# Optimization experiments

Hardware: AMD Instinct MI355X
Metric: run time of the kernel (lower is better)

The kernel has to match this reference:

```python
import jax, jax.numpy as jnp
import numpy as np

N_NODES = 50000


def gcn_conv(h, W, b, src, dst, n_nodes):
    # PyG GCNConv: h' = D^{-1/2} (A + I) D^{-1/2} (h @ W) + b
    h = h @ W  # [N, out]
    deg = jax.ops.segment_sum(jnp.ones_like(dst, dtype=h.dtype), dst, num_segments=n_nodes)
    dinv = jnp.where(deg > 0, jax.lax.rsqrt(deg), 0.0)  # [N]
    norm = dinv[src] * dinv[dst]  # [E]
    msg = h[src] * norm[:, None]  # [E, out]
    out = jax.ops.segment_sum(msg, dst, num_segments=n_nodes)
    return out + b


def setup_inputs() -> dict:
    key = jax.random.key(0)
    ks = jax.random.split(key, 12)
    N, E, P, D, H = N_NODES, 1600000, 200000, 128, 128
    s = lambda fan_in: 1.0 / np.sqrt(fan_in)
    return {
        "x": jax.random.normal(ks[0], (N, D), dtype=jnp.float32),
        "edge_index": jax.random.randint(ks[1], (2, E), 0, N, dtype=jnp.int32),
        "drug_pairs": jax.random.randint(ks[2], (P, 2), 0, N, dtype=jnp.int32),
        "W1": jax.random.normal(ks[3], (D, H), dtype=jnp.float32) * s(D),
        "b1": jnp.zeros((H,), dtype=jnp.float32),
        "W2": jax.random.normal(ks[4], (H, H), dtype=jnp.float32) * s(H),
        "b2": jnp.zeros((H,), dtype=jnp.float32),
        "Wh1": jax.random.normal(ks[5], (2 * H, H), dtype=jnp.float32) * s(2 * H),
        "bh1": jnp.zeros((H,), dtype=jnp.float32),
        "Wh2": jax.random.normal(ks[6], (H, 1), dtype=jnp.float32) * s(H),
        "bh2": jnp.zeros((1,), dtype=jnp.float32),
    }


def reference(x, edge_index, drug_pairs, W1, b1, W2, b2, Wh1, bh1, Wh2, bh2):
    n = x.shape[0]
    # add self-loops once (GCNConv default add_self_loops=True)
    loop = jnp.arange(n, dtype=edge_index.dtype)
    src = jnp.concatenate([edge_index[0], loop])
    dst = jnp.concatenate([edge_index[1], loop])

    h = jax.nn.relu(gcn_conv(x, W1, b1, src, dst, n))  # dropout = identity (eval)
    h = jax.nn.relu(gcn_conv(h, W2, b2, src, dst, n))

    combined = jnp.concatenate([h[drug_pairs[:, 0]], h[drug_pairs[:, 1]]], axis=1)  # [P, 2H]
    out = jax.nn.relu(combined @ Wh1 + bh1) @ Wh2 + bh2  # [P, 1]
    return out
```

## Files before the change

kernel.cpp:

```cpp
#include <hip/hip_runtime.h>
#include <hip/hip_fp16.h>


#define BSH 9
#define BSZ (1 << BSH)
#define MSB 4096
#define XPAD 132
#define HB 256

typedef __attribute__((ext_vector_type(8))) short bf16x8;
typedef __attribute__((ext_vector_type(8))) _Float16 f16x8;
typedef __attribute__((ext_vector_type(4))) float f32x4;

__device__ __forceinline__ void acc8(uint4 u, float4& lo, float4& hi) {
  float2 f0 = __half22float2(((const __half2*)&u)[0]);
  float2 f1 = __half22float2(((const __half2*)&u)[1]);
  float2 f2 = __half22float2(((const __half2*)&u)[2]);
  float2 f3 = __half22float2(((const __half2*)&u)[3]);
  lo.x += f0.x; lo.y += f0.y; lo.z += f1.x; lo.w += f1.y;
  hi.x += f2.x; hi.y += f2.y; hi.z += f3.x; hi.w += f3.y;
}

__device__ __forceinline__ void split8(const float* v, bf16x8& hi, bf16x8& lo) {
#pragma unroll
  for (int j = 0; j < 8; ++j) {
    unsigned u = __float_as_uint(v[j]);
    hi[j] = (short)(u >> 16);
    float lf = v[j] - __uint_as_float(u & 0xffff0000u);
    lo[j] = (short)(__float_as_uint(lf) >> 16);
  }
}

__global__ __launch_bounds__(256) void k_prep_hist(
    const float* __restrict__ W1, const float* __restrict__ W2,
    const float* __restrict__ Wh1, short* __restrict__ fragH,
    short* __restrict__ fragL,
    const int* __restrict__ dst, int* __restrict__ gcnt, int e, int kb) {
  if (blockIdx.x >= 32) {
    __shared__ int h4[512];
    int bid = blockIdx.x - 32;
    int tid = threadIdx.x, wid = tid >> 6;
    for (int t = tid; t < 512; t += 256) h4[t] = 0;
    __syncthreads();
    for (int i = bid * 256 + tid; i < e; i += HB * 256) {
      int d = __builtin_nontemporal_load(&dst[i]);
      atomicAdd(&h4[wid * 128 + (d >> BSH)], 1);
    }
    __syncthreads();
    if (tid < kb)
      atomicAdd(&gcnt[tid], h4[tid] + h4[128 + tid] + h4[256 + tid] + h4[384 + tid]);
    return;
  }
  int g = blockIdx.x * 256 + threadIdx.x;
  int w = g >> 11;
  int rem = g & 2047;
  int lane = rem & 63;
  int ts = rem >> 6;
  int t = ts >> 2, s = ts & 3;
  int n = (t << 4) + (lane & 15);
  int k0 = s * 32 + (lane >> 4) * 8;
  const float* W = (w == 0) ? W1 : (w == 1) ? W2 : (w == 2) ? Wh1 : (Wh1 + 128 * 128);
  short h[8], l[8];
#pragma unroll
  for (int j = 0; j < 8; ++j) {
    float x = W[(k0 + j) * 128 + n];
    if (w == 0) {
      unsigned u = __float_as_uint(x);
      h[j] = (short)(u >> 16);
      float lf = x - __uint_as_float(u & 0xffff0000u);
      l[j] = (short)(__float_as_uint(lf) >> 16);
    } else {
      __half hh = __float2half(x);
      h[j] = __half_as_short(hh);
      l[j] = __half_as_short(__float2half(x - __half2float(hh)));
    }
  }
  ((int4*)fragH)[g] = *(int4*)h;
  ((int4*)fragL)[g] = *(int4*)l;
}

__global__ __launch_bounds__(256) void k_gemm_mfma(
    const float* __restrict__ X, const short* __restrict__ fragH,
    const short* __restrict__ fragL, const float* __restrict__ rowscale,
    __half* __restrict__ C16, int n) {
  __shared__ float sX[64 * XPAD];
  int tid = threadIdx.x;
  int row0 = blockIdx.x * 64;
  const float2* X2 = (const float2*)(X + (size_t)row0 * 128);
#pragma unroll
  for (int it = 0; it < 16; ++it) {
    int t = it * 256 + tid;
    int r = t >> 6, c2 = t & 63;
    int gr = row0 + r;
    float2 v = (gr < n) ? X2[t] : make_float2(0.f, 0.f);
    *(float2*)&sX[r * XPAD + c2 * 2] = v;
  }
  __syncthreads();
  int wid = tid >> 6, lane = tid & 63;
  int r0 = row0 + wid * 16;
  if (r0 >= n) return;
  int m = lane & 15, quad = lane >> 4;
  const float* xrow = sX + (wid * 16 + m) * XPAD;
  f32x4 acc[8];
#pragma unroll
  for (int t = 0; t < 8; ++t) acc[t] = (f32x4)(0.f);
  const int4* FH = (const int4*)fragH;
  const int4* FL = (const int4*)fragL;
#pragma unroll
  for (int s = 0; s < 4; ++s) {
    int k0 = s * 32 + quad * 8;
    float xv[8];
    *(float2*)&xv[0] = *(const float2*)(xrow + k0);
    *(float2*)&xv[2] = *(const float2*)(xrow + k0 + 2);
    *(float2*)&xv[4] = *(const float2*)(xrow + k0 + 4);
    *(float2*)&xv[6] = *(const float2*)(xrow + k0 + 6);
    bf16x8 ah, al;
    split8(xv, ah, al);
#pragma unroll
    for (int t = 0; t < 8; ++t) {
      int idx = (t * 4 + s) * 64 + lane;
      bf16x8 bh = *(const bf16x8*)&FH[idx];
      bf16x8 bl = *(const bf16x8*)&FL[idx];
      acc[t] = __builtin_amdgcn_mfma_f32_16x16x32_bf16(ah, bh, acc[t], 0, 0, 0);
      acc[t] = __builtin_amdgcn_mfma_f32_16x16x32_bf16(al, bh, acc[t], 0, 0, 0);
      acc[t] = __builtin_amdgcn_mfma_f32_16x16x32_bf16(ah, bl, acc[t], 0, 0, 0);
    }
  }
  float sc[4];
#pragma unroll
  for (int r = 0; r < 4; ++r)
    sc[r] = rowscale[r0 + quad * 4 + r];
#pragma unroll
  for (int t = 0; t < 8; ++t) {
#pragma unroll
    for (int r = 0; r < 4; ++r) {
      int row = r0 + quad * 4 + r;
      C16[(size_t)row * 128 + t * 16 + m] = __float2half(acc[t][r] * sc[r]);
    }
  }
}

__global__ __launch_bounds__(256) void k_gemm_f16(
    const __half* __restrict__ X16, const short* __restrict__ fragH,
    const short* __restrict__ fragL, const float* __restrict__ rowscale,
    __half* __restrict__ C16, int n) {
  int wid = threadIdx.x >> 6, lane = threadIdx.x & 63;
  int r0 = (blockIdx.x * 4 + wid) * 16;
  if (r0 >= n) return;
  int m = lane & 15, quad = lane >> 4;
  const uint4* Xr = (const uint4*)(X16 + (size_t)(r0 + m) * 128);
  f32x4 acc[8];
#pragma unroll
  for (int t = 0; t < 8; ++t) acc[t] = (f32x4)(0.f);
  const int4* FH = (const int4*)fragH;
  const int4* FL = (const int4*)fragL;
#pragma unroll
  for (int s = 0; s < 4; ++s) {
    uint4 av = Xr[quad + 4 * s];
    f16x8 a = *(const f16x8*)&av;
#pragma unroll
    for (int t = 0; t < 8; ++t) {
      int idx = (t * 4 + s) * 64 + lane;
      int4 bhv = FH[idx], blv = FL[idx];
      f16x8 bh = *(const f16x8*)&bhv;
      f16x8 bl = *(const f16x8*)&blv;
      acc[t] = __builtin_amdgcn_mfma_f32_16x16x32_f16(a, bh, acc[t], 0, 0, 0);
      acc[t] = __builtin_amdgcn_mfma_f32_16x16x32_f16(a, bl, acc[t], 0, 0, 0);
    }
  }
  float sc[4];
#pragma unroll
  for (int r = 0; r < 4; ++r)
    sc[r] = rowscale ? rowscale[r0 + quad * 4 + r] : 1.f;
#pragma unroll
  for (int t = 0; t < 8; ++t) {
#pragma unroll
    for (int r = 0; r < 4; ++r) {
      int row = r0 + quad * 4 + r;
      C16[(size_t)row * 128 + t * 16 + m] = __float2half(acc[t][r] * sc[r]);
    }
  }
}

__global__ __launch_bounds__(256) void k_gemm_dual_f16(
    const __half* __restrict__ X16,
    const short* __restrict__ fHa, const short* __restrict__ fLa,
    const short* __restrict__ fHb, const short* __restrict__ fLb,
    __half* __restrict__ A16, __half* __restrict__ B16, int n) {
  int wid = threadIdx.x >> 6, lane = threadIdx.x & 63;
  int r0 = (blockIdx.x * 4 + wid) * 16;
  if (r0 >= n) return;
  int m = lane & 15, quad = lane >> 4;
  const uint4* Xr = (const uint4*)(X16 + (size_t)(r0 + m) * 128);
  f32x4 accA[8], accB[8];
#pragma unroll
  for (int t = 0; t < 8; ++t) { accA[t] = (f32x4)(0.f); accB[t] = (f32x4)(0.f); }
  const int4* FHa = (const int4*)fHa; const int4* FLa = (const int4*)fLa;
  const int4* FHb = (const int4*)fHb; const int4* FLb = (const int4*)fLb;
#pragma unroll
  for (int s = 0; s < 4; ++s) {
    uint4 av = Xr[quad + 4 * s];
    f16x8 a = *(const f16x8*)&av;
#pragma unroll
    for (int t = 0; t < 8; ++t) {
      int idx = (t * 4 + s) * 64 + lane;
      int4 v0 = FHa[idx], v1 = FLa[idx], v2 = FHb[idx], v3 = FLb[idx];
      accA[t] = __builtin_amdgcn_mfma_f32_16x16x32_f16(a, *(const f16x8*)&v0, accA[t], 0, 0, 0);
      accA[t] = __builtin_amdgcn_mfma_f32_16x16x32_f16(a, *(const f16x8*)&v1, accA[t], 0, 0, 0);
      accB[t] = __builtin_amdgcn_mfma_f32_16x16x32_f16(a, *(const f16x8*)&v2, accB[t], 0, 0, 0);
      accB[t] = __builtin_amdgcn_mfma_f32_16x16x32_f16(a, *(const f16x8*)&v3, accB[t], 0, 0, 0);
    }
  }
#pragma unroll
  for (int t = 0; t < 8; ++t) {
#pragma unroll
    for (int r = 0; r < 4; ++r) {
      int row = r0 + quad * 4 + r;
      A16[(size_t)row * 128 + t * 16 + m] = __float2half(accA[t][r]);
      B16[(size_t)row * 128 + t * 16 + m] = __float2half(accB[t][r]);
    }
  }
}

__global__ __launch_bounds__(256) void k_multisplit(const int* __restrict__ src,
                                                    const int* __restrict__ dst,
                                                    const int* __restrict__ gcnt,
                                                    int* __restrict__ gcur,
                                                    int* __restrict__ tmp,
                                                    int e, int kb) {
  __shared__ int h4[4 * 128], off[4 * 128], sbase[128], ws[2];
  int tid = threadIdx.x, wid = tid >> 6, lane = tid & 63;
  for (int t = tid; t < 512; t += 256) h4[t] = 0;
  __syncthreads();
  int i0 = blockIdx.x * MSB + tid;
  int d[16], rk[16];
#pragma unroll
  for (int u = 0; u < 16; ++u) {
    int i = i0 + u * 256;
    if (i < e) {
      d[u] = __builtin_nontemporal_load(&dst[i]);
      rk[u] = atomicAdd(&h4[wid * 128 + (d[u] >> BSH)], 1);
    }
  }
  __syncthreads();
  int tot = 0;
  if (tid < 128) {
    int c0 = h4[tid], c1 = h4[128 + tid], c2 = h4[256 + tid], c3 = h4[384 + tid];
    off[tid] = 0; off[128 + tid] = c0;
    off[256 + tid] = c0 + c1; off[384 + tid] = c0 + c1 + c2;
    tot = c0 + c1 + c2 + c3;
  }
  int v = (tid < 128 && tid < kb) ? gcnt[tid] : 0;
  int orig = v;
#pragma unroll
  for (int o = 1; o < 64; o <<= 1) {
    int u = __shfl_up(v, o, 64);
    if (lane >= o) v += u;
  }
  if (lane == 63 && wid < 2) ws[wid] = v;
  __syncthreads();
  if (tid < 128) sbase[tid] = ((wid == 1) ? ws[0] : 0) + v - orig;
  __syncthreads();
  if (tid < kb && tot > 0) sbase[tid] += atomicAdd(&gcur[tid], tot);
  __syncthreads();
#pragma unroll
  for (int u = 0; u < 16; ++u) {
    int i = i0 + u * 256;
    if (i < e) {
      int s = __builtin_nontemporal_load(&src[i]);
      int k = d[u] >> BSH;
      tmp[sbase[k] + off[wid * 128 + k] + rk[u]] = ((d[u] & (BSZ - 1)) << 16) | s;
    }
  }
}

__global__ __launch_bounds__(512) void k_bucket_build(
    const int* __restrict__ tmp, const int* __restrict__ gcnt,
    int* __restrict__ rowptr, float* __restrict__ dinv,
    unsigned short* __restrict__ colarr, int n, int kb, int e) {
  __shared__ int dl[BSZ], cl[BSZ], sbase[128], ws[8];
  int t = threadIdx.x, b = blockIdx.x;
  int lane = t & 63, w = t >> 6;
  int v = (t < 128 && t < kb) ? gcnt[t] : 0;
  int orig0 = v;
#pragma unroll
  for (int o = 1; o < 64; o <<= 1) {
    int u = __shfl_up(v, o, 64);
    if (lane >= o) v += u;
  }
  if (lane == 63 && w < 2) ws[w] = v;
  dl[t] = 0;
  __syncthreads();
  if (t < 128) sbase[t] = ((w == 1) ? ws[0] : 0) + v - orig0;
  __syncthreads();
  int s0 = sbase[b];
  int s1 = s0 + gcnt[b];
  for (int j = s0 + t; j < s1; j += 512)
    atomicAdd(&dl[((unsigned)tmp[j]) >> 16], 1);
  __syncthreads();
  int dv = dl[t], orig = dv;
#pragma unroll
  for (int o = 1; o < 64; o <<= 1) {
    int u = __shfl_up(dv, o, 64);
    if (lane >= o) dv += u;
  }
  if (lane == 63) ws[w] = dv;
  __syncthreads();
  if (t == 0) {
    int a = 0;
#pragma unroll
    for (int k = 0; k < 8; ++k) { int x = ws[k]; ws[k] = a; a += x; }
  }
  __syncthreads();
  int ex = ws[w] + dv - orig;
  cl[t] = ex;
  int node = (b << BSH) + t;
  if (node < n) {
    rowptr[node] = s0 + ex;
    dinv[node] = rsqrtf((float)(orig + 1));
  }
  if (b == kb - 1 && t == 0) rowptr[n] = e;
  __syncthreads();
  for (int j = s0 + t; j < s1; j += 512) {
    int p = tmp[j];
    int r = atomicAdd(&cl[((unsigned)p) >> 16], 1);
    colarr[s0 + r] = (unsigned short)(p & 0xFFFF);
  }
}

__global__ __launch_bounds__(256) void k_agg_h(
    const __half2* __restrict__ g2, const float* __restrict__ dinv,
    const int* __restrict__ rowptr, const unsigned short* __restrict__ col,
    const float* __restrict__ bias, __half* __restrict__ out16, int n) {
  int i = blockIdx.x * 4 + (threadIdx.x >> 6);
  if (i >= n) return;
  int lane = threadIdx.x & 63;
  int sub = lane >> 4;
  int c8 = lane & 15;
  const uint4* G = (const uint4*)g2;
  float4 z = make_float4(0.f, 0.f, 0.f, 0.f);
  float4 lo0 = z, lo1 = z, lo2 = z, lo3 = z, hi0 = z, hi1 = z, hi2 = z, hi3 = z;
  if (sub == 0) acc8(G[(size_t)i * 16 + c8], lo0, hi0);
  int beg = rowptr[i], end = rowptr[i + 1];
  int j = beg;
  for (; j + 16 <= end; j += 16) {
    int s0 = __builtin_nontemporal_load(&col[j + sub]);
    int s1 = __builtin_nontemporal_load(&col[j + 4 + sub]);
    int s2 = __builtin_nontemporal_load(&col[j + 8 + sub]);
    int s3 = __builtin_nontemporal_load(&col[j + 12 + sub]);
    uint4 u0 = G[(size_t)s0 * 16 + c8];
    uint4 u1 = G[(size_t)s1 * 16 + c8];
    uint4 u2 = G[(size_t)s2 * 16 + c8];
    uint4 u3 = G[(size_t)s3 * 16 + c8];
    acc8(u0, lo0, hi0); acc8(u1, lo1, hi1);
    acc8(u2, lo2, hi2); acc8(u3, lo3, hi3);
  }
  for (; j + 4 <= end; j += 4) {
    int s0 = __builtin_nontemporal_load(&col[j + sub]);
    acc8(G[(size_t)s0 * 16 + c8], lo1, hi1);
  }
  int rem = end - j;
  if (sub < rem) {
    int s0 = __builtin_nontemporal_load(&col[j + sub]);
    acc8(G[(size_t)s0 * 16 + c8], lo2, hi2);
  }
  float4 lo, hi;
  lo.x = (lo0.x + lo1.x) + (lo2.x + lo3.x);
  lo.y = (lo0.y + lo1.y) + (lo2.y + lo3.y);
  lo.z = (lo0.z + lo1.z) + (lo2.z + lo3.z);
  lo.w = (lo0.w + lo1.w) + (lo2.w + lo3.w);
  hi.x = (hi0.x + hi1.x) + (hi2.x + hi3.x);
  hi.y = (hi0.y + hi1.y) + (hi2.y + hi3.y);
  hi.z = (hi0.z + hi1.z) + (hi2.z + hi3.z);
  hi.w = (hi0.w + hi1.w) + (hi2.w + hi3.w);
  lo.x += __shfl_down(lo.x, 32, 64); lo.x += __shfl_down(lo.x, 16, 64);
  lo.y += __shfl_down(lo.y, 32, 64); lo.y += __shfl_down(lo.y, 16, 64);
  lo.z += __shfl_down(lo.z, 32, 64); lo.z += __shfl_down(lo.z, 16, 64);
  lo.w += __shfl_down(lo.w, 32, 64); lo.w += __shfl_down(lo.w, 16, 64);
  hi.x += __shfl_down(hi.x, 32, 64); hi.x += __shfl_down(hi.x, 16, 64);
  hi.y += __shfl_down(hi.y, 32, 64); hi.y += __shfl_down(hi.y, 16, 64);
  hi.z += __shfl_down(hi.z, 32, 64); hi.z += __shfl_down(hi.z, 16, 64);
  hi.w += __shfl_down(hi.w, 32, 64); hi.w += __shfl_down(hi.w, 16, 64);
  if (sub == 0) {
    float di = dinv[i];
    float4 b0 = ((const float4*)bias)[2 * c8];
    float4 b1 = ((const float4*)bias)[2 * c8 + 1];
    __half2 q0 = __floats2half2_rn(fmaxf(fmaf(di, lo.x, b0.x), 0.f),
                                   fmaxf(fmaf(di, lo.y, b0.y), 0.f));
    __half2 q1 = __floats2half2_rn(fmaxf(fmaf(di, lo.z, b0.z), 0.f),
                                   fmaxf(fmaf(di, lo.w, b0.w), 0.f));
    __half2 q2 = __floats2half2_rn(fmaxf(fmaf(di, hi.x, b1.x), 0.f),
                                   fmaxf(fmaf(di, hi.y, b1.y), 0.f));
    __half2 q3 = __floats2half2_rn(fmaxf(fmaf(di, hi.z, b1.z), 0.f),
                                   fmaxf(fmaf(di, hi.w, b1.w), 0.f));
    uint4 o;
    o.x = *(unsigned*)&q0; o.y = *(unsigned*)&q1;
    o.z = *(unsigned*)&q2; o.w = *(unsigned*)&q3;
    ((uint4*)out16)[(size_t)i * 16 + c8] = o;
  }
}

__global__ __launch_bounds__(256) void k_pairs_h(
    const __half* __restrict__ A, const __half* __restrict__ B,
    const int* __restrict__ pairs, const float* __restrict__ bh1,
    const float* __restrict__ wh2, const float* __restrict__ bh2,
    float* __restrict__ out, int P) {
  int wp = (blockIdx.x * 4 + (threadIdx.x >> 6)) * 4;
  int lane = threadIdx.x & 63;
  int sub = lane >> 4;
  int c8 = lane & 15;
  int pr = sub >> 1;
  int ab = sub & 1;
  const uint4* T = ab ? (const uint4*)B : (const uint4*)A;
  int pA = wp + pr;
  int pB = wp + 2 + pr;
  uint4 u0 = make_uint4(0, 0, 0, 0), u1 = u0;
  if (pA < P) {
    int r = pairs[2 * pA + ab];
    u0 = T[(size_t)r * 16 + c8];
  }
  if (pB < P) {
    int r = pairs[2 * pB + ab];
    u1 = T[(size_t)r * 16 + c8];
  }
  float4 b0 = ((const float4*)bh1)[2 * c8];
  float4 b1 = ((const float4*)bh1)[2 * c8 + 1];
  float4 w0 = ((const float4*)wh2)[2 * c8];
  float4 w1 = ((const float4*)wh2)[2 * c8 + 1];
  float s0, s1;
  {
    float4 lo = make_float4(0, 0, 0, 0), hi = lo;
    acc8(u0, lo, hi);
    lo.x += __shfl_down(lo.x, 16, 64); lo.y += __shfl_down(lo.y, 16, 64);
    lo.z += __shfl_down(lo.z, 16, 64); lo.w += __shfl_down(lo.w, 16, 64);
    hi.x += __shfl_down(hi.x, 16, 64); hi.y += __shfl_down(hi.y, 16, 64);
    hi.z += __shfl_down(hi.z, 16, 64); hi.w += __shfl_down(hi.w, 16, 64);
    s0 = fmaxf(lo.x + b0.x, 0.f) * w0.x + fmaxf(lo.y + b0.y, 0.f) * w0.y +
         fmaxf(lo.z + b0.z, 0.f) * w0.z + fmaxf(lo.w + b0.w, 0.f) * w0.w +
         fmaxf(hi.x + b1.x, 0.f) * w1.x + fmaxf(hi.y + b1.y, 0.f) * w1.y +
         fmaxf(hi.z + b1.z, 0.f) * w1.z + fmaxf(hi.w + b1.w, 0.f) * w1.w;
  }
  {
    float4 lo = make_float4(0, 0, 0, 0), hi = lo;
    acc8(u1, lo, hi);
    lo.x += __shfl_down(lo.x, 16, 64); lo.y += __shfl_down(lo.y, 16, 64);
    lo.z += __shfl_down(lo.z, 16, 64); lo.w += __shfl_down(lo.w, 16, 64);
    hi.x += __shfl_down(hi.x, 16, 64); hi.y += __shfl_down(hi.y, 16, 64);
    hi.z += __shfl_down(hi.z, 16, 64); hi.w += __shfl_down(hi.w, 16, 64);
    s1 = fmaxf(lo.x + b0.x, 0.f) * w0.x + fmaxf(lo.y + b0.y, 0.f) * w0.y +
         fmaxf(lo.z + b0.z, 0.f) * w0.z + fmaxf(lo.w + b0.w, 0.f) * w0.w +
         fmaxf(hi.x + b1.x, 0.f) * w1.x + fmaxf(hi.y + b1.y, 0.f) * w1.y +
         fmaxf(hi.z + b1.z, 0.f) * w1.z + fmaxf(hi.w + b1.w, 0.f) * w1.w;
  }
#pragma unroll
  for (int o = 8; o > 0; o >>= 1) {
    s0 += __shfl_down(s0, o, 64);
    s1 += __shfl_down(s1, o, 64);
  }
  float bb = bh2[0];
  if (lane == 0 && wp < P) out[wp] = s0 + bb;
  if (lane == 32 && wp + 1 < P) out[wp + 1] = s0 + bb;
  if (lane == 0 && wp + 2 < P) out[wp + 2] = s1 + bb;
  if (lane == 32 && wp + 3 < P) out[wp + 3] = s1 + bb;
}

extern "C" void kernel_launch(void* const* d_in, const int* in_sizes, int n_in,
                              void* d_out, int out_size, void* d_ws, size_t ws_size,
                              hipStream_t stream) {
  const float* x   = (const float*)d_in[0];
  const int* ei    = (const int*)d_in[1];
  const int* pairs = (const int*)d_in[2];
  const float* W1  = (const float*)d_in[3];
  const float* b1  = (const float*)d_in[4];
  const float* W2  = (const float*)d_in[5];
  const float* b2  = (const float*)d_in[6];
  const float* Wh1 = (const float*)d_in[7];
  const float* bh1 = (const float*)d_in[8];
  const float* Wh2 = (const float*)d_in[9];
  const float* bh2 = (const float*)d_in[10];
  (void)n_in; (void)out_size; (void)ws_size;

  int N = in_sizes[0] / 128;
  int E = in_sizes[1] / 2;
  int P = in_sizes[2] / 2;
  const int* src = ei;
  const int* dst = ei + E;
  int KB = (N + BSZ - 1) >> BSH;

  char* wsp = (char*)d_ws;
  size_t off = 0;
  auto alloc = [&](size_t bytes) -> void* {
    void* p = wsp + off;
    off += (bytes + 255) & ~(size_t)255;
    return p;
  };
  __half* g16 = (__half*)alloc((size_t)N * 128 * 2);
  __half* h1  = (__half*)alloc((size_t)N * 128 * 2);
  __half* h2  = (__half*)alloc((size_t)N * 128 * 2);
  float* dinv = (float*)alloc((size_t)N * 4);
  int* rowptr = (int*)alloc((size_t)(N + 1) * 4);
  unsigned short* colarr = (unsigned short*)alloc((size_t)E * 2);
  int* tmp    = (int*)alloc((size_t)E * 4);
  short* fragH = (short*)alloc(4 * 2048 * 8 * 2);
  short* fragL = (short*)alloc(4 * 2048 * 8 * 2);
  int* gcnt  = (int*)alloc((size_t)(KB + 1) * 4);
  int* gcur  = (int*)alloc((size_t)(KB + 1) * 4);
  __half* A16 = g16;
  __half* B16 = h1;
  short* fH_W1 = fragH + 0 * 16384;  short* fL_W1 = fragL + 0 * 16384;
  short* fH_W2 = fragH + 1 * 16384;  short* fL_W2 = fragL + 1 * 16384;
  short* fH_Wa = fragH + 2 * 16384;  short* fL_Wa = fragL + 2 * 16384;
  short* fH_Wb = fragH + 3 * 16384;  short* fL_Wb = fragL + 3 * 16384;

  int GB = (N + 63) / 64;
  int GF = (N / 16 + 3) / 4;
  int AB = (N + 3) / 4;

  hipMemsetAsync(gcnt, 0, (size_t)(KB + 1) * 4, stream);
  hipMemsetAsync(gcur, 0, (size_t)(KB + 1) * 4, stream);
  k_prep_hist<<<32 + HB, 256, 0, stream>>>(W1, W2, Wh1, fragH, fragL,
                                           dst, gcnt, E, KB);
  k_multisplit<<<(E + MSB - 1) / MSB, 256, 0, stream>>>(src, dst, gcnt, gcur,
                                                        tmp, E, KB);
  k_bucket_build<<<KB, 512, 0, stream>>>(tmp, gcnt, rowptr, dinv, colarr, N, KB, E);
  k_gemm_mfma<<<GB, 256, 0, stream>>>(x, fH_W1, fL_W1, dinv, g16, N);
  k_agg_h<<<AB, 256, 0, stream>>>((const __half2*)g16, dinv, rowptr, colarr, b1, h1, N);
  k_gemm_f16<<<GF, 256, 0, stream>>>(h1, fH_W2, fL_W2, dinv, g16, N);
  k_agg_h<<<AB, 256, 0, stream>>>((const __half2*)g16, dinv, rowptr, colarr, b2, h2, N);
  k_gemm_dual_f16<<<GF, 256, 0, stream>>>(h2, fH_Wa, fL_Wa, fH_Wb, fL_Wb,
                                          A16, B16, N);
  k_pairs_h<<<(P + 15) / 16, 256, 0, stream>>>(A16, B16, pairs, bh1, Wh2, bh2,
                                               (float*)d_out, P);
}
```

Before: 353.2 us.

## Co-launch multisplit with first GEMM and apply dinv scaling in separate pass

Merges the edge multisplit kernel and the first-layer GEMM into one launch, with the block index choosing which body runs, so the GEMM no longer waits for the CSR build. Because dinv is not yet known at GEMM time, the row scaling moves to a new elementwise kernel that runs after the bucket build. The GEMM writes its output in fp16 before scaling and the new pass rounds it again, which can change numerics slightly. The extra pass also rereads and rewrites the 50000x128 fp16 buffer, and the two memsets are merged into one.

```diff
diff --git a/kernel.cpp b/kernel.cpp
--- a/kernel.cpp
+++ b/kernel.cpp
@@ -79,13 +79,12 @@
   ((int4*)fragL)[g] = *(int4*)l;
 }
 
-__global__ __launch_bounds__(256) void k_gemm_mfma(
+__device__ __forceinline__ void gemm1_body(
     const float* __restrict__ X, const short* __restrict__ fragH,
-    const short* __restrict__ fragL, const float* __restrict__ rowscale,
-    __half* __restrict__ C16, int n) {
-  __shared__ float sX[64 * XPAD];
+    const short* __restrict__ fragL, __half* __restrict__ C16, int n,
+    int bid, float* sX) {
   int tid = threadIdx.x;
-  int row0 = blockIdx.x * 64;
+  int row0 = bid * 64;
   const float2* X2 = (const float2*)(X + (size_t)row0 * 128);
 #pragma unroll
   for (int it = 0; it < 16; ++it) {
@@ -126,18 +125,151 @@
       acc[t] = __builtin_amdgcn_mfma_f32_16x16x32_bf16(ah, bl, acc[t], 0, 0, 0);
     }
   }
-  float sc[4];
-#pragma unroll
-  for (int r = 0; r < 4; ++r)
-    sc[r] = rowscale[r0 + quad * 4 + r];
 #pragma unroll
   for (int t = 0; t < 8; ++t) {
 #pragma unroll
     for (int r = 0; r < 4; ++r) {
       int row = r0 + quad * 4 + r;
-      C16[(size_t)row * 128 + t * 16 + m] = __float2half(acc[t][r] * sc[r]);
-    }
-  }
+      C16[(size_t)row * 128 + t * 16 + m] = __float2half(acc[t][r]);
+    }
+  }
+}
+
+__device__ __forceinline__ void multisplit_body(
+    const int* __restrict__ src, const int* __restrict__ dst,
+    const int* __restrict__ gcnt, int* __restrict__ gcur,
+    int* __restrict__ tmp, int e, int kb, int bid, int* lds) {
+  int* h4 = lds;
+  int* off = lds + 512;
+  int* sbase = lds + 1024;
+  int* ws = lds + 1152;
+  int tid = threadIdx.x, wid = tid >> 6, lane = tid & 63;
+  for (int t = tid; t < 512; t += 256) h4[t] = 0;
+  __syncthreads();
+  int i0 = bid * MSB + tid;
+  int d[16], rk[16];
+#pragma unroll
+  for (int u = 0; u < 16; ++u) {
+    int i = i0 + u * 256;
+    if (i < e) {
+      d[u] = __builtin_nontemporal_load(&dst[i]);
+      rk[u] = atomicAdd(&h4[wid * 128 + (d[u] >> BSH)], 1);
+    }
+  }
+  __syncthreads();
+  int tot = 0;
+  if (tid < 128) {
+    int c0 = h4[tid], c1 = h4[128 + tid], c2 = h4[256 + tid], c3 = h4[384 + tid];
+    off[tid] = 0; off[128 + tid] = c0;
+    off[256 + tid] = c0 + c1; off[384 + tid] = c0 + c1 + c2;
+    tot = c0 + c1 + c2 + c3;
+  }
+  int v = (tid < 128 && tid < kb) ? gcnt[tid] : 0;
+  int orig = v;
+#pragma unroll
+  for (int o = 1; o < 64; o <<= 1) {
+    int u = __shfl_up(v, o, 64);
+    if (lane >= o) v += u;
+  }
+  if (lane == 63 && wid < 2) ws[wid] = v;
+  __syncthreads();
+  if (tid < 128) sbase[tid] = ((wid == 1) ? ws[0] : 0) + v - orig;
+  __syncthreads();
+  if (tid < kb && tot > 0) sbase[tid] += atomicAdd(&gcur[tid], tot);
+  __syncthreads();
+#pragma unroll
+  for (int u = 0; u < 16; ++u) {
+    int i = i0 + u * 256;
+    if (i < e) {
+      int s = __builtin_nontemporal_load(&src[i]);
+      int k = d[u] >> BSH;
+      tmp[sbase[k] + off[wid * 128 + k] + rk[u]] = ((d[u] & (BSZ - 1)) << 16) | s;
+    }
+  }
+}
+
+__global__ __launch_bounds__(256) void k_ms_gemm1(
+    const int* __restrict__ src, const int* __restrict__ dst,
+    const int* __restrict__ gcnt, int* __restrict__ gcur,
+    int* __restrict__ tmp, int e, int kb, int msblocks,
+    const float* __restrict__ X, const short* __restrict__ fragH,
+    const short* __restrict__ fragL, __half* __restrict__ C16, int n) {
+  __shared__ float sX[64 * XPAD];
+  if ((int)blockIdx.x < msblocks) {
+    multisplit_body(src, dst, gcnt, gcur, tmp, e, kb, blockIdx.x, (int*)sX);
+    return;
+  }
+  gemm1_body(X, fragH, fragL, C16, n, blockIdx.x - msblocks, sX);
+}
+
+__global__ __launch_bounds__(512) void k_bucket_build(
+    const int* __restrict__ tmp, const int* __restrict__ gcnt,
+    int* __restrict__ rowptr, float* __restrict__ dinv,
+    unsigned short* __restrict__ colarr, int n, int kb, int e) {
+  __shared__ int dl[BSZ], cl[BSZ], sbase[128], ws[8];
+  int t = threadIdx.x, b = blockIdx.x;
+  int lane = t & 63, w = t >> 6;
+  int v = (t < 128 && t < kb) ? gcnt[t] : 0;
+  int orig0 = v;
+#pragma unroll
+  for (int o = 1; o < 64; o <<= 1) {
+    int u = __shfl_up(v, o, 64);
+    if (lane >= o) v += u;
+  }
+  if (lane == 63 && w < 2) ws[w] = v;
+  dl[t] = 0;
+  __syncthreads();
+  if (t < 128) sbase[t] = ((w == 1) ? ws[0] : 0) + v - orig0;
+  __syncthreads();
+  int s0 = sbase[b];
+  int s1 = s0 + gcnt[b];
+  for (int j = s0 + t; j < s1; j += 512)
+    atomicAdd(&dl[((unsigned)tmp[j]) >> 16], 1);
+  __syncthreads();
+  int dv = dl[t], orig = dv;
+#pragma unroll
+  for (int o = 1; o < 64; o <<= 1) {
+    int u = __shfl_up(dv, o, 64);
+    if (lane >= o) dv += u;
+  }
+  if (lane == 63) ws[w] = dv;
+  __syncthreads();
+  if (t == 0) {
+    int a = 0;
+#pragma unroll
+    for (int k = 0; k < 8; ++k) { int x = ws[k]; ws[k] = a; a += x; }
+  }
+  __syncthreads();
+  int ex = ws[w] + dv - orig;
+  cl[t] = ex;
+  int node = (b << BSH) + t;
+  if (node < n) {
+    rowptr[node] = s0 + ex;
+    dinv[node] = rsqrtf((float)(orig + 1));
+  }
+  if (b == kb - 1 && t == 0) rowptr[n] = e;
+  __syncthreads();
+  for (int j = s0 + t; j < s1; j += 512) {
+    int p = tmp[j];
+    int r = atomicAdd(&cl[((unsigned)p) >> 16], 1);
+    colarr[s0 + r] = (unsigned short)(p & 0xFFFF);
+  }
+}
+
+__global__ __launch_bounds__(256) void k_gscale(__half* __restrict__ g16,
+                                                const float* __restrict__ dinv,
+                                                int n) {
+  int idx = blockIdx.x * 256 + threadIdx.x;
+  if (idx >= n * 16) return;
+  float di = dinv[idx >> 4];
+  uint4 u = ((const uint4*)g16)[idx];
+  __half2* hp = (__half2*)&u;
+#pragma unroll
+  for (int k = 0; k < 4; ++k) {
+    float2 f = __half22float2(hp[k]);
+    hp[k] = __floats2half2_rn(f.x * di, f.y * di);
+  }
+  ((uint4*)g16)[idx] = u;
 }
 
 __global__ __launch_bounds__(256) void k_gemm_f16(
@@ -219,112 +351,6 @@
       A16[(size_t)row * 128 + t * 16 + m] = __float2half(accA[t][r]);
       B16[(size_t)row * 128 + t * 16 + m] = __float2half(accB[t][r]);
     }
-  }
-}
-
-__global__ __launch_bounds__(256) void k_multisplit(const int* __restrict__ src,
-                                                    const int* __restrict__ dst,
-                                                    const int* __restrict__ gcnt,
-                                                    int* __restrict__ gcur,
-                                                    int* __restrict__ tmp,
-                                                    int e, int kb) {
-  __shared__ int h4[4 * 128], off[4 * 128], sbase[128], ws[2];
-  int tid = threadIdx.x, wid = tid >> 6, lane = tid & 63;
-  for (int t = tid; t < 512; t += 256) h4[t] = 0;
-  __syncthreads();
-  int i0 = blockIdx.x * MSB + tid;
-  int d[16], rk[16];
-#pragma unroll
-  for (int u = 0; u < 16; ++u) {
-    int i = i0 + u * 256;
-    if (i < e) {
-      d[u] = __builtin_nontemporal_load(&dst[i]);
-      rk[u] = atomicAdd(&h4[wid * 128 + (d[u] >> BSH)], 1);
-    }
-  }
-  __syncthreads();
-  int tot = 0;
-  if (tid < 128) {
-    int c0 = h4[tid], c1 = h4[128 + tid], c2 = h4[256 + tid], c3 = h4[384 + tid];
-    off[tid] = 0; off[128 + tid] = c0;
-    off[256 + tid] = c0 + c1; off[384 + tid] = c0 + c1 + c2;
-    tot = c0 + c1 + c2 + c3;
-  }
-  int v = (tid < 128 && tid < kb) ? gcnt[tid] : 0;
-  int orig = v;
-#pragma unroll
-  for (int o = 1; o < 64; o <<= 1) {
-    int u = __shfl_up(v, o, 64);
-    if (lane >= o) v += u;
-  }
-  if (lane == 63 && wid < 2) ws[wid] = v;
-  __syncthreads();
-  if (tid < 128) sbase[tid] = ((wid == 1) ? ws[0] : 0) + v - orig;
-  __syncthreads();
-  if (tid < kb && tot > 0) sbase[tid] += atomicAdd(&gcur[tid], tot);
-  __syncthreads();
-#pragma unroll
-  for (int u = 0; u < 16; ++u) {
-    int i = i0 + u * 256;
-    if (i < e) {
-      int s = __builtin_nontemporal_load(&src[i]);
-      int k = d[u] >> BSH;
-      tmp[sbase[k] + off[wid * 128 + k] + rk[u]] = ((d[u] & (BSZ - 1)) << 16) | s;
-    }
-  }
-}
-
-__global__ __launch_bounds__(512) void k_bucket_build(
-    const int* __restrict__ tmp, const int* __restrict__ gcnt,
-    int* __restrict__ rowptr, float* __restrict__ dinv,
-    unsigned short* __restrict__ colarr, int n, int kb, int e) {
-  __shared__ int dl[BSZ], cl[BSZ], sbase[128], ws[8];
-  int t = threadIdx.x, b = blockIdx.x;
-  int lane = t & 63, w = t >> 6;
-  int v = (t < 128 && t < kb) ? gcnt[t] : 0;
-  int orig0 = v;
-#pragma unroll
-  for (int o = 1; o < 64; o <<= 1) {
-    int u = __shfl_up(v, o, 64);
-    if (lane >= o) v += u;
-  }
-  if (lane == 63 && w < 2) ws[w] = v;
-  dl[t] = 0;
-  __syncthreads();
-  if (t < 128) sbase[t] = ((w == 1) ? ws[0] : 0) + v - orig0;
-  __syncthreads();
-  int s0 = sbase[b];
-  int s1 = s0 + gcnt[b];
-  for (int j = s0 + t; j < s1; j += 512)
-    atomicAdd(&dl[((unsigned)tmp[j]) >> 16], 1);
-  __syncthreads();
-  int dv = dl[t], orig = dv;
-#pragma unroll
-  for (int o = 1; o < 64; o <<= 1) {
-    int u = __shfl_up(dv, o, 64);
-    if (lane >= o) dv += u;
-  }
-  if (lane == 63) ws[w] = dv;
-  __syncthreads();
-  if (t == 0) {
-    int a = 0;
-#pragma unroll
-    for (int k = 0; k < 8; ++k) { int x = ws[k]; ws[k] = a; a += x; }
-  }
-  __syncthreads();
-  int ex = ws[w] + dv - orig;
-  cl[t] = ex;
-  int node = (b << BSH) + t;
-  if (node < n) {
-    rowptr[node] = s0 + ex;
-    dinv[node] = rsqrtf((float)(orig + 1));
-  }
-  if (b == kb - 1 && t == 0) rowptr[n] = e;
-  __syncthreads();
-  for (int j = s0 + t; j < s1; j += 512) {
-    int p = tmp[j];
-    int r = atomicAdd(&cl[((unsigned)p) >> 16], 1);
-    colarr[s0 + r] = (unsigned short)(p & 0xFFFF);
   }
 }
 
@@ -503,8 +529,9 @@
   int* tmp    = (int*)alloc((size_t)E * 4);
   short* fragH = (short*)alloc(4 * 2048 * 8 * 2);
   short* fragL = (short*)alloc(4 * 2048 * 8 * 2);
-  int* gcnt  = (int*)alloc((size_t)(KB + 1) * 4);
-  int* gcur  = (int*)alloc((size_t)(KB + 1) * 4);
+  int* gc     = (int*)alloc(2 * 128 * 4);
+  int* gcnt = gc;
+  int* gcur = gc + 128;
   __half* A16 = g16;
   __half* B16 = h1;
   short* fH_W1 = fragH + 0 * 16384;  short* fL_W1 = fragL + 0 * 16384;
@@ -515,15 +542,15 @@
   int GB = (N + 63) / 64;
   int GF = (N / 16 + 3) / 4;
   int AB = (N + 3) / 4;
-
-  hipMemsetAsync(gcnt, 0, (size_t)(KB + 1) * 4, stream);
-  hipMemsetAsync(gcur, 0, (size_t)(KB + 1) * 4, stream);
+  int MS = (E + MSB - 1) / MSB;
+
+  hipMemsetAsync(gc, 0, 2 * 128 * 4, stream);
   k_prep_hist<<<32 + HB, 256, 0, stream>>>(W1, W2, Wh1, fragH, fragL,
                                            dst, gcnt, E, KB);
-  k_multisplit<<<(E + MSB - 1) / MSB, 256, 0, stream>>>(src, dst, gcnt, gcur,
-                                                        tmp, E, KB);
+  k_ms_gemm1<<<MS + GB, 256, 0, stream>>>(src, dst, gcnt, gcur, tmp, E, KB, MS,
+                                          x, fH_W1, fL_W1, g16, N);
   k_bucket_build<<<KB, 512, 0, stream>>>(tmp, gcnt, rowptr, dinv, colarr, N, KB, E);
-  k_gemm_mfma<<<GB, 256, 0, stream>>>(x, fH_W1, fL_W1, dinv, g16, N);
+  k_gscale<<<(N * 16 + 255) / 256, 256, 0, stream>>>(g16, dinv, N);
   k_agg_h<<<AB, 256, 0, stream>>>((const __half2*)g16, dinv, rowptr, colarr, b1, h1, N);
   k_gemm_f16<<<GF, 256, 0, stream>>>(h1, fH_W2, fL_W2, dinv, g16, N);
   k_agg_h<<<AB, 256, 0, stream>>>((const __half2*)g16, dinv, rowptr, colarr, b2, h2, N);
```

After: 349.2 us. About the same (-1.1%).
